# Kernel tuning notes

Measured on AMD Instinct MI355X. Metric: run time of the kernel, lower is better.

Reference implementation:

```python
import jax, jax.numpy as jnp
import numpy as np

B, T, CIN, F, K, U, FF, N, LS = 16, 384, 64, 64, 32, 128, 1024, 64, 15
EPS = 1e-3  # keras BatchNormalization epsilon

def _conv1d(x, w):
    # x:[B,T,C], w:[K,C,F], 'same' padding, no bias
    return jax.lax.conv_general_dilated(x, w, (1,), 'SAME', dimension_numbers=('NWC', 'WIO', 'NWC'))

def _bn(x, g, b, m, v):
    # inference-mode batchnorm
    return g * (x - m) * jax.lax.rsqrt(v + EPS) + b

def _gru_seq(x, k, rk, b):
    # keras GRU (reset_after=True), gate order [z, r, h]; x:[B,T,D] -> [B,T,U]
    u = rk.shape[0]
    xp = x @ k + b[0]                      # precompute input projections [B,T,3U]
    def step(h, xt):
        rec = h @ rk + b[1]
        xz, xr, xh = jnp.split(xt, 3, axis=-1)
        rz, rr_, rh = jnp.split(rec, 3, axis=-1)
        z = jax.nn.sigmoid(xz + rz)
        r = jax.nn.sigmoid(xr + rr_)
        hh = jnp.tanh(xh + r * rh)
        hn = z * h + (1.0 - z) * hh
        return hn, hn
    h0 = jnp.zeros((x.shape[0], u), x.dtype)
    _, ys = jax.lax.scan(step, h0, jnp.swapaxes(xp, 0, 1))
    return jnp.swapaxes(ys, 0, 1)

def _cgru(xr, xi, kr, rkr, br, ki, rki, bi):
    # ComplexGRUCell: real_gru applied to both parts, imag_gru applied to both parts
    rr = _gru_seq(xr, kr, rkr, br)
    ri = _gru_seq(xi, kr, rkr, br)
    ir = _gru_seq(xr, ki, rki, bi)
    ii = _gru_seq(xi, ki, rki, bi)
    return rr - ii, ri + ir

def _forward(h_real, h_imag, conv_wr, conv_wi, bn_gr, bn_br, bn_mr, bn_vr, bn_gi, bn_bi, bn_mi, bn_vi, g0_kr, g0_rkr, g0_br, g0_ki, g0_rki, g0_bi, gs_kr, gs_rkr, gs_br, gs_ki, gs_rki, gs_bi, ff1_w, ff1_b, ff2_w, ff2_b, qr_w, qr_b, qi_w, qi_b, rr_w, rr_b, ri_w, ri_b):
    xr = _bn(_conv1d(h_real, conv_wr) - _conv1d(h_imag, conv_wi), bn_gr, bn_br, bn_mr, bn_vr)
    xi = _bn(_conv1d(h_imag, conv_wr) + _conv1d(h_real, conv_wi), bn_gi, bn_bi, bn_mi, bn_vi)
    xr, xi = _cgru(xr, xi, g0_kr, g0_rkr, g0_br, g0_ki, g0_rki, g0_bi)
    for i in range(LS):  # fixed small layer count
        xr, xi = _cgru(xr, xi, gs_kr[i], gs_rkr[i], gs_br[i], gs_ki[i], gs_rki[i], gs_bi[i])
    def ff(a):
        return jax.nn.relu(a @ ff1_w + ff1_b) @ ff2_w + ff2_b
    xr = xr + ff(xr)   # dropout is identity at inference
    xi = xi + ff(xi)
    mr = jnp.mean(xr, axis=1)
    mi = jnp.mean(xi, axis=1)
    Qr = (mr @ qr_w + qr_b) - (mi @ qi_w + qi_b)
    Qi = (mi @ qr_w + qr_b) + (mr @ qi_w + qi_b)
    Rr = (mr @ rr_w + rr_b) - (mi @ ri_w + ri_b)
    Ri = (mi @ rr_w + rr_b) + (mr @ ri_w + ri_b)
    Qr = Qr.reshape(-1, N, N); Qi = Qi.reshape(-1, N, N)
    Rr = Rr.reshape(-1, N, N); Ri = Ri.reshape(-1, N, N)
    # trace(Q Q^H) = sum |Q|^2 (real, nonnegative)
    nrm = jnp.sqrt(jnp.sum(Qr * Qr + Qi * Qi, axis=(1, 2)))[:, None, None]
    scale = jnp.sqrt(jnp.float32(N)) / nrm
    return Qr * scale, Qi * scale, Rr, Ri

def setup_inputs():
    key = jax.random.key(0)
    ks = jax.random.split(key, 20)
    s = 0.05
    def nrm(k, shape, scale=s):
        return jax.random.normal(k, shape, jnp.float32) * scale
    inp = {}
    inp['h_real'] = nrm(ks[0], (B, T, CIN), 1.0)
    inp['h_imag'] = nrm(ks[1], (B, T, CIN), 1.0)
    inp['conv_wr'] = nrm(ks[2], (K, CIN, F))
    inp['conv_wi'] = nrm(ks[3], (K, CIN, F))
    for nm in ('bn_gr', 'bn_gi', 'bn_vr', 'bn_vi'):
        inp[nm] = jnp.ones((F,), jnp.float32)
    for nm in ('bn_br', 'bn_bi', 'bn_mr', 'bn_mi'):
        inp[nm] = jnp.zeros((F,), jnp.float32)
    inp['g0_kr'] = nrm(ks[4], (F, 3 * U));  inp['g0_rkr'] = nrm(ks[5], (U, 3 * U));  inp['g0_br'] = jnp.zeros((2, 3 * U), jnp.float32)
    inp['g0_ki'] = nrm(ks[6], (F, 3 * U));  inp['g0_rki'] = nrm(ks[7], (U, 3 * U));  inp['g0_bi'] = jnp.zeros((2, 3 * U), jnp.float32)
    inp['gs_kr'] = nrm(ks[8], (LS, U, 3 * U));  inp['gs_rkr'] = nrm(ks[9], (LS, U, 3 * U));  inp['gs_br'] = jnp.zeros((LS, 2, 3 * U), jnp.float32)
    inp['gs_ki'] = nrm(ks[10], (LS, U, 3 * U)); inp['gs_rki'] = nrm(ks[11], (LS, U, 3 * U)); inp['gs_bi'] = jnp.zeros((LS, 2, 3 * U), jnp.float32)
    inp['ff1_w'] = nrm(ks[12], (U, FF)); inp['ff1_b'] = jnp.zeros((FF,), jnp.float32)
    inp['ff2_w'] = nrm(ks[13], (FF, U)); inp['ff2_b'] = jnp.zeros((U,), jnp.float32)
    inp['qr_w'] = nrm(ks[14], (U, N * N)); inp['qr_b'] = jnp.zeros((N * N,), jnp.float32)
    inp['qi_w'] = nrm(ks[15], (U, N * N)); inp['qi_b'] = jnp.zeros((N * N,), jnp.float32)
    inp['rr_w'] = nrm(ks[16], (U, N * N)); inp['rr_b'] = jnp.zeros((N * N,), jnp.float32)
    inp['ri_w'] = nrm(ks[17], (U, N * N)); inp['ri_b'] = jnp.zeros((N * N,), jnp.float32)
    return inp

def reference(h_real, h_imag, conv_wr, conv_wi, bn_gr, bn_br, bn_mr, bn_vr, bn_gi, bn_bi, bn_mi, bn_vi, g0_kr, g0_rkr, g0_br, g0_ki, g0_rki, g0_bi, gs_kr, gs_rkr, gs_br, gs_ki, gs_rki, gs_bi, ff1_w, ff1_b, ff2_w, ff2_b, qr_w, qr_b, qi_w, qi_b, rr_w, rr_b, ri_w, ri_b):
    return _forward(h_real, h_imag, conv_wr, conv_wi, bn_gr, bn_br, bn_mr, bn_vr, bn_gi, bn_bi, bn_mi, bn_vi, g0_kr, g0_rkr, g0_br, g0_ki, g0_rki, g0_bi, gs_kr, gs_rkr, gs_br, gs_ki, gs_rki, gs_bi, ff1_w, ff1_b, ff2_w, ff2_b, qr_w, qr_b, qi_w, qi_b, rr_w, rr_b, ri_w, ri_b)
```

## Files before the change

kernel.cpp:

```cpp
#include <hip/hip_runtime.h>
#include <hip/hip_bf16.h>
#include <math.h>

typedef __attribute__((ext_vector_type(8))) short short8;
typedef __attribute__((ext_vector_type(4))) float f32x4;
typedef unsigned short u16;
typedef unsigned int u32;

#define CL 16
#define NCHUNK 24
#define RING 4
#define CHSZ (16*CL*128)

__device__ __forceinline__ u16 f2bf(float f){
  u32 x = __float_as_uint(f);
  u32 r = x + 0x7fffu + ((x >> 16) & 1u);
  return (u16)(r >> 16);
}
__device__ __forceinline__ float bf2f(u16 u){
  return __uint_as_float(((u32)u) << 16);
}
__device__ __forceinline__ f32x4 mfma16(short8 a, short8 b, f32x4 c){
  return __builtin_amdgcn_mfma_f32_16x16x32_bf16(a, b, c, 0, 0, 0);
}

__global__ void k_init(float* S, float* ssq, u32* Flg){
  int i = blockIdx.x*256 + threadIdx.x;
  if (i < 32768){ S[i] = 0.f; return; }
  i -= 32768;
  if (i < 16){ ssq[i] = 0.f; return; }
  i -= 16;
  if (i < 4096){ Flg[i] = 0u; return; }
}

__global__ void k_wprep(const float* __restrict__ wr, const float* __restrict__ wi,
                        const float* __restrict__ w1,
                        u16* WtR, u16* WtI, u16* WtIN, u16* W1t){
  int i = blockIdx.x*256 + threadIdx.x;
  if (i < 131072){
    int k = i >> 12, r = i & 4095, f = r >> 6, c = r & 63;
    float a = wr[(k<<12) + (c<<6) + f];
    float b = wi[(k<<12) + (c<<6) + f];
    WtR[i] = f2bf(a); WtI[i] = f2bf(b); WtIN[i] = f2bf(-b);
  } else if (i < 262144){
    int j = i - 131072;
    int col = j >> 7, k = j & 127;
    W1t[j] = f2bf(w1[(k<<10) + col]);
  }
}

__global__ __launch_bounds__(256) void k_wprep2(
    const float* __restrict__ g0_kr, const float* __restrict__ g0_ki,
    const float* __restrict__ gs_kr, const float* __restrict__ gs_ki,
    const float* __restrict__ g0_rkr, const float* __restrict__ g0_rki,
    const float* __restrict__ gs_rkr, const float* __restrict__ gs_rki,
    u16* __restrict__ KT, u16* __restrict__ RKT){
  __shared__ float tile[128][33];
  int bid = blockIdx.x;
  int ct = bid % 12; int lm = (bid/12) & 31; int which = bid / (12*32);
  int m = lm & 1, l = lm >> 1;
  int c0 = ct*32;
  int tid = threadIdx.x;
  for (int idx = tid; idx < 128*32; idx += 256){
    int k = idx >> 5, cc = idx & 31;
    float v;
    if (!which){
      if (l == 0) v = (k < 64) ? (m ? g0_ki : g0_kr)[k*384 + c0+cc] : 0.f;
      else        v = (m ? gs_ki : gs_kr)[((size_t)(l-1)*128 + k)*384 + c0+cc];
    } else {
      if (l == 0) v = (m ? g0_rki : g0_rkr)[k*384 + c0+cc];
      else        v = (m ? gs_rki : gs_rkr)[((size_t)(l-1)*128 + k)*384 + c0+cc];
    }
    tile[k][cc] = v;
  }
  __syncthreads();
  u16* dst = (which ? RKT : KT) + (size_t)lm*384*128;
  for (int idx = tid; idx < 32*128; idx += 256){
    int cc = idx >> 7, k = idx & 127;
    dst[(size_t)(c0+cc)*128 + k] = f2bf(tile[k][cc]);
  }
}

__global__ __launch_bounds__(256) void k_conv(
    const float* __restrict__ hr, const float* __restrict__ hi,
    const u16* __restrict__ WtR, const u16* __restrict__ WtI, const u16* __restrict__ WtIN,
    const float* __restrict__ gr, const float* __restrict__ gi,
    const float* __restrict__ vr, const float* __restrict__ vi,
    const float* __restrict__ br, const float* __restrict__ bi,
    const float* __restrict__ mr, const float* __restrict__ mi,
    u16* __restrict__ X0){
  __shared__ u16 xst[2*48*64];
  int tid = threadIdx.x;
  int bid = blockIdx.x;
  int b = bid / 24, t0 = (bid % 24) * 16;
  for (int el = tid; el < 2*47*64; el += 256){
    int part = el / (47*64); int rem = el % (47*64); int row = rem >> 6; int c = rem & 63;
    int tg = t0 + row - 15;
    const float* src = part ? hi : hr;
    float v = (tg >= 0 && tg < 384) ? src[((size_t)b*384 + tg)*64 + c] : 0.f;
    int idx = (part*48 + row)*64 + c;
    int byte = (idx<<1) ^ ((row&7)<<4);
    *(u16*)((char*)xst + byte) = f2bf(v);
  }
  __syncthreads();
  int lane = tid & 63, wid = tid >> 6, lr = lane & 15, lg = lane >> 4;
  f32x4 accr = {0,0,0,0}, acci = {0,0,0,0};
  for (int k = 0; k < 32; ++k){
    int row = lr + k;
    int swz = (row&7)<<4;
    for (int ch = 0; ch < 2; ++ch){
      int c0 = ch*32 + lg*8;
      int idxr = (0*48 + row)*64 + c0;
      int idxi = (1*48 + row)*64 + c0;
      short8 ar = *(const short8*)((const char*)xst + ((idxr<<1) ^ swz));
      short8 ai = *(const short8*)((const char*)xst + ((idxi<<1) ^ swz));
      size_t wb = ((size_t)(k*64 + wid*16 + lr))*64 + c0;
      short8 bwr = *(const short8*)(WtR + wb);
      short8 bwi = *(const short8*)(WtI + wb);
      short8 bwn = *(const short8*)(WtIN + wb);
      accr = mfma16(ar, bwr, accr);
      accr = mfma16(ai, bwn, accr);
      acci = mfma16(ai, bwr, acci);
      acci = mfma16(ar, bwi, acci);
    }
  }
  int f = wid*16 + lr;
  float sr_ = gr[f] * rsqrtf(vr[f] + 1e-3f), or_ = br[f] - mr[f]*sr_;
  float si_ = gi[f] * rsqrtf(vi[f] + 1e-3f), oi_ = bi[f] - mi[f]*si_;
  for (int r = 0; r < 4; ++r){
    int t = t0 + lg*4 + r;
    X0[(((size_t)0*16 + b)*384 + t)*64 + f] = f2bf(accr[r]*sr_ + or_);
    X0[(((size_t)1*16 + b)*384 + t)*64 + f] = f2bf(acci[r]*si_ + oi_);
  }
}

__global__ __launch_bounds__(512,1) void k_scanp(
    const u16* __restrict__ X0, const u16* __restrict__ KT, const u16* __restrict__ RKT,
    const float* __restrict__ g0_br, const float* __restrict__ g0_bi,
    const float* __restrict__ gs_br, const float* __restrict__ gs_bi,
    u16* __restrict__ HC, u16* __restrict__ HS15, u32* Flg)
{
  int bid = blockIdx.x;
  int l = bid >> 2, s = bid & 3;

  __shared__ u16 xs[16*CL*128];
  __shared__ u16 hs2[2*16*128];
  __shared__ float bsh[4][128];

  int tid = threadIdx.x, lane = tid & 63, wv = tid >> 6, lr = lane & 15, lg = lane >> 4;
  int m = s >> 1;

  const float* Bsrc = (l == 0) ? (m ? g0_bi : g0_br)
                               : ((m ? gs_bi : gs_br) + (size_t)(l-1)*768);
  if (tid < 128){
    int j = tid;
    bsh[0][j] = Bsrc[j]       + Bsrc[384 + j];
    bsh[1][j] = Bsrc[128 + j] + Bsrc[384 + 128 + j];
    bsh[2][j] = Bsrc[256 + j];
    bsh[3][j] = Bsrc[384 + 256 + j];
  }
  for (int i = tid; i < 2048; i += 512) ((u32*)hs2)[i] = 0u;

  const u16* Kp  = KT  + (size_t)(l*2 + m)*384*128;
  const u16* RKp = RKT + (size_t)(l*2 + m)*384*128;
  int cz = wv*16 + lr;
  short8 wz[8], wr2[8], whx[4], whr[4];
  #pragma unroll
  for (int ks = 0; ks < 4; ++ks){
    wz[ks]    = *(const short8*)(RKp + (size_t)cz*128 + ks*32 + lg*8);
    wz[4+ks]  = *(const short8*)(Kp  + (size_t)cz*128 + ks*32 + lg*8);
    wr2[ks]   = *(const short8*)(RKp + (size_t)(128+cz)*128 + ks*32 + lg*8);
    wr2[4+ks] = *(const short8*)(Kp  + (size_t)(128+cz)*128 + ks*32 + lg*8);
    whx[ks]   = *(const short8*)(Kp  + (size_t)(256+cz)*128 + ks*32 + lg*8);
    whr[ks]   = *(const short8*)(RKp + (size_t)(256+cz)*128 + ks*32 + lg*8);
  }

  float hreg[4] = {0.f, 0.f, 0.f, 0.f};

  __syncthreads();
  float bz, br_, bhx, bhr;
  {
    int j = wv*16 + lr;
    bz = bsh[0][j]; br_ = bsh[1][j]; bhx = bsh[2][j]; bhr = bsh[3][j];
  }

  u32* prodF = Flg;
  u32* consF = Flg + 2048;
  int sA = (s & 1) ? 1 : 0, sB = (s & 1) ? 2 : 3;
  int pA = (l-1)*4 + sA, pB = (l-1)*4 + sB;
  float sgn = (s & 1) ? 1.f : -1.f;
  int p = s & 1;
  int me = l*4 + s;

  for (int c = 0; c < NCHUNK; ++c){
    int t0 = c * CL;

    if (tid == 0){
      int guard = 0;
      if (l > 0){
        while (__hip_atomic_load(&prodF[pA*32], __ATOMIC_RELAXED, __HIP_MEMORY_SCOPE_AGENT) < (u32)(c+1) ||
               __hip_atomic_load(&prodF[pB*32], __ATOMIC_RELAXED, __HIP_MEMORY_SCOPE_AGENT) < (u32)(c+1)){
          __builtin_amdgcn_s_sleep(1);
          if (++guard > 10000000) break;
        }
      }
      if (l < 15 && c >= RING){
        guard = 0;
        while (__hip_atomic_load(&consF[me*32], __ATOMIC_RELAXED, __HIP_MEMORY_SCOPE_AGENT) < (u32)(2*(c-RING+1))){
          __builtin_amdgcn_s_sleep(1);
          if (++guard > 10000000) break;
        }
      }
    }
    __syncthreads();

    if (l == 0){
      for (int it = 0; it < 8; ++it){
        int g = tid + it*512;
        int k8 = g & 15, ttv = (g>>4) & 15, b = g >> 8;
        short8 v = {0,0,0,0,0,0,0,0};
        if (k8 < 8) v = *(const short8*)(X0 + (((size_t)p*16 + b)*384 + t0 + ttv)*64 + k8*8);
        int byte = (((b*CL + ttv)*128 + k8*8) << 1) ^ ((b&7)<<4);
        *(short8*)((char*)xs + byte) = v;
      }
      __syncthreads();
    } else {
      __builtin_amdgcn_fence(__ATOMIC_ACQUIRE, "agent");
      int slot = c & (RING-1);
      const u16* baseA = HC + ((size_t)pA*RING + slot)*CHSZ;
      const u16* baseB = HC + ((size_t)pB*RING + slot)*CHSZ;
      for (int it = 0; it < 8; ++it){
        int g = tid + it*512;
        int k8 = g & 15, ttv = (g>>4) & 15, b = g >> 8;
        size_t si = ((size_t)b*CL + ttv)*128 + k8*8;
        short8 va = *(const short8*)(baseA + si);
        short8 vb = *(const short8*)(baseB + si);
        short8 o;
        #pragma unroll
        for (int e = 0; e < 8; ++e){
          float f = bf2f((u16)va[e]) + sgn*bf2f((u16)vb[e]);
          o[e] = (short)f2bf(f);
        }
        int byte = (((b*CL + ttv)*128 + k8*8) << 1) ^ ((b&7)<<4);
        *(short8*)((char*)xs + byte) = o;
      }
      __syncthreads();
      if (tid == 0){
        __hip_atomic_fetch_add(&consF[pA*32], 1u, __ATOMIC_RELAXED, __HIP_MEMORY_SCOPE_AGENT);
        __hip_atomic_fetch_add(&consF[pB*32], 1u, __ATOMIC_RELAXED, __HIP_MEMORY_SCOPE_AGENT);
      }
    }

    u16* outp;
    int Tp, tbase;
    if (l < 15){
      outp = HC + ((size_t)me*RING + (c & (RING-1)))*CHSZ;
      Tp = CL; tbase = 0;
    } else {
      outp = HS15 + (size_t)s*16*384*128;
      Tp = 384; tbase = t0;
    }

    for (int q = 0; q < 4; ++q){
      f32x4 xpz[4], xpr[4], xph[4];
      #pragma unroll
      for (int t2 = 0; t2 < 4; ++t2){
        int tt = q*4 + t2;
        short8 ax[4];
        #pragma unroll
        for (int ks = 0; ks < 4; ++ks){
          int xb = (((lr*CL + tt)*128 + ks*32 + lg*8) << 1) ^ ((lr&7)<<4);
          ax[ks] = *(const short8*)((char*)xs + xb);
        }
        f32x4 az  = {bz, bz, bz, bz};
        f32x4 ar  = {br_, br_, br_, br_};
        f32x4 ahx = {bhx, bhx, bhx, bhx};
        #pragma unroll
        for (int ks = 0; ks < 4; ++ks){
          az  = mfma16(ax[ks], wz[4+ks],  az);
          ar  = mfma16(ax[ks], wr2[4+ks], ar);
          ahx = mfma16(ax[ks], whx[ks],   ahx);
        }
        xpz[t2] = az; xpr[t2] = ar; xph[t2] = ahx;
      }
      #pragma unroll
      for (int t2 = 0; t2 < 4; ++t2){
        int tt = q*4 + t2;
        int hp = tt & 1;
        short8 ah[4];
        #pragma unroll
        for (int ks = 0; ks < 4; ++ks){
          int hb = hp*4096 + (((lr*128 + ks*32 + lg*8) << 1) ^ ((lr&7)<<4));
          ah[ks] = *(const short8*)((char*)hs2 + hb);
        }
        f32x4 az  = xpz[t2];
        f32x4 ar  = xpr[t2];
        f32x4 ahr = {bhr, bhr, bhr, bhr};
        #pragma unroll
        for (int ks = 0; ks < 4; ++ks){
          az  = mfma16(ah[ks], wz[ks],  az);
          ar  = mfma16(ah[ks], wr2[ks], ar);
          ahr = mfma16(ah[ks], whr[ks], ahr);
        }
        int j = wv*16 + lr;
        #pragma unroll
        for (int r = 0; r < 4; ++r){
          int b = lg*4 + r;
          float z  = 1.f/(1.f + __expf(-az[r]));
          float rg = 1.f/(1.f + __expf(-ar[r]));
          float pre = xph[t2][r] + rg*ahr[r];
          pre = fminf(fmaxf(pre, -15.f), 15.f);
          float e2 = __expf(2.f*pre);
          float hh = (e2 - 1.f)/(e2 + 1.f);
          float hn = z*hreg[r] + (1.f - z)*hh;
          hreg[r] = hn;
          u16 hb16 = f2bf(hn);
          int byte = ((hp^1)*4096) + ((((b*128 + j) << 1)) ^ ((b&7)<<4));
          *(u16*)((char*)hs2 + byte) = hb16;
          outp[((size_t)b*Tp + tbase + tt)*128 + j] = hb16;
        }
        __syncthreads();
      }
    }

    if (l < 15 && tid == 0){
      __hip_atomic_fetch_add(&prodF[me*32], 1u, __ATOMIC_RELEASE, __HIP_MEMORY_SCOPE_AGENT);
    }
  }
}

__global__ __launch_bounds__(256) void k_ffs(const u16* __restrict__ HS, const u16* __restrict__ W1t,
                                             const float* __restrict__ b1, float* __restrict__ S){
  int bid = blockIdx.x;
  int part = bid / 384; int rem = bid % 384;
  int b = rem / 24; int rem2 = rem % 24;
  int t0 = (rem2 / 4) * 64, c0 = (rem2 % 4) * 256;
  int tid = threadIdx.x, lane = tid & 63, wid = tid >> 6, lr = lane & 15, lg = lane >> 4;
  int sA = part ? 1 : 0, sB = part ? 2 : 3;
  float sgn = part ? 1.f : -1.f;
  short8 af[4][4];
  #pragma unroll
  for (int rt = 0; rt < 4; ++rt)
    #pragma unroll
    for (int ks = 0; ks < 4; ++ks){
      size_t i1 = (((size_t)sA*16 + b)*384 + t0 + rt*16 + lr)*128 + ks*32 + lg*8;
      size_t i2 = (((size_t)sB*16 + b)*384 + t0 + rt*16 + lr)*128 + ks*32 + lg*8;
      short8 va = *(const short8*)(HS + i1);
      short8 vb = *(const short8*)(HS + i2);
      short8 o;
      #pragma unroll
      for (int e = 0; e < 8; ++e){
        float f = bf2f((u16)va[e]) + sgn*bf2f((u16)vb[e]);
        o[e] = (short)f2bf(f);
      }
      af[rt][ks] = o;
    }
  for (int ctl = 0; ctl < 4; ++ctl){
    int col = c0 + wid*64 + ctl*16 + lr;
    short8 bf[4];
    #pragma unroll
    for (int ks = 0; ks < 4; ++ks)
      bf[ks] = *(const short8*)(W1t + (size_t)col*128 + ks*32 + lg*8);
    float bias = b1[col];
    float ssum = 0.f;
    #pragma unroll
    for (int rt = 0; rt < 4; ++rt){
      f32x4 acc = {0,0,0,0};
      #pragma unroll
      for (int ks = 0; ks < 4; ++ks) acc = mfma16(af[rt][ks], bf[ks], acc);
      #pragma unroll
      for (int r = 0; r < 4; ++r) ssum += fmaxf(acc[r] + bias, 0.f);
    }
    ssum += __shfl_xor(ssum, 16, 64);
    ssum += __shfl_xor(ssum, 32, 64);
    if (lg == 0) atomicAdd(&S[((size_t)part*16 + b)*1024 + col], ssum);
  }
}

__global__ void k_mx(const u16* __restrict__ HS, float* __restrict__ Mx){
  int pb = blockIdx.x; int u = threadIdx.x;
  int p = pb >> 4, b = pb & 15;
  int sA = p ? 1 : 0, sB = p ? 2 : 3;
  float sgn = p ? 1.f : -1.f;
  float s = 0.f;
  for (int t = 0; t < 384; ++t){
    float a = bf2f(HS[(((size_t)sA*16 + b)*384 + t)*128 + u]);
    float c = bf2f(HS[(((size_t)sB*16 + b)*384 + t)*128 + u]);
    s += a + sgn*c;
  }
  Mx[pb*128 + u] = s;
}

__global__ void k_comb(const float* __restrict__ S, const float* __restrict__ Mx,
                       const float* __restrict__ w2, const float* __restrict__ b2,
                       float* __restrict__ M){
  int pb = blockIdx.x; int u = threadIdx.x;
  const float* Sp = S + (size_t)pb*1024;
  float acc = 0.f;
  for (int f = 0; f < 1024; ++f) acc += Sp[f] * w2[(size_t)f*128 + u];
  M[pb*128 + u] = Mx[pb*128 + u] * (1.f/384.f) + acc * (1.f/384.f) + b2[u];
}

__global__ __launch_bounds__(256) void k_qr(const float* __restrict__ M,
    const float* __restrict__ qr_w, const float* __restrict__ qr_b,
    const float* __restrict__ qi_w, const float* __restrict__ qi_b,
    const float* __restrict__ rr_w, const float* __restrict__ rr_b,
    const float* __restrict__ ri_w, const float* __restrict__ ri_b,
    float* __restrict__ out, float* __restrict__ ssq){
  __shared__ float smr[128], smi[128];
  int bid = blockIdx.x; int tid = threadIdx.x;
  int b = bid >> 4; int o = (bid & 15)*256 + tid;
  if (tid < 128){ smr[tid] = M[b*128 + tid]; smi[tid] = M[(16 + b)*128 + tid]; }
  __syncthreads();
  float aq=0, bq=0, cq=0, dq=0, ar=0, br2=0, cr=0, dr=0;
  for (int u = 0; u < 128; ++u){
    float mr = smr[u], mi = smi[u];
    float wqr = qr_w[(size_t)u*4096 + o], wqi = qi_w[(size_t)u*4096 + o];
    float wrr = rr_w[(size_t)u*4096 + o], wri = ri_w[(size_t)u*4096 + o];
    aq += mr*wqr;  bq += mi*wqi;  cq += mi*wqr;  dq += mr*wqi;
    ar += mr*wrr;  br2 += mi*wri; cr += mi*wrr;  dr += mr*wri;
  }
  float Qr = (aq + qr_b[o]) - (bq + qi_b[o]);
  float Qi = (cq + qr_b[o]) + (dq + qi_b[o]);
  float Rr = (ar + rr_b[o]) - (br2 + ri_b[o]);
  float Ri = (cr + rr_b[o]) + (dr + ri_b[o]);
  out[(size_t)b*4096 + o] = Qr;
  out[65536 + (size_t)b*4096 + o] = Qi;
  out[131072 + (size_t)b*4096 + o] = Rr;
  out[196608 + (size_t)b*4096 + o] = Ri;
  float ss = Qr*Qr + Qi*Qi;
  for (int off = 32; off; off >>= 1) ss += __shfl_down(ss, off, 64);
  if ((tid & 63) == 0) atomicAdd(&ssq[b], ss);
}

__global__ void k_scale(float* __restrict__ out, const float* __restrict__ ssq){
  int i = blockIdx.x*256 + threadIdx.x;
  int b = (i >> 12) & 15;
  float s = 8.f / sqrtf(ssq[b]);
  out[i] *= s;
}

extern "C" void kernel_launch(void* const* d_in, const int* in_sizes, int n_in,
                              void* d_out, int out_size, void* d_ws, size_t ws_size,
                              hipStream_t stream){
  const float* h_real = (const float*)d_in[0];
  const float* h_imag = (const float*)d_in[1];
  const float* conv_wr = (const float*)d_in[2];
  const float* conv_wi = (const float*)d_in[3];
  const float* bn_gr = (const float*)d_in[4];
  const float* bn_gi = (const float*)d_in[5];
  const float* bn_vr = (const float*)d_in[6];
  const float* bn_vi = (const float*)d_in[7];
  const float* bn_br = (const float*)d_in[8];
  const float* bn_bi = (const float*)d_in[9];
  const float* bn_mr = (const float*)d_in[10];
  const float* bn_mi = (const float*)d_in[11];
  const float* g0_kr = (const float*)d_in[12];
  const float* g0_rkr = (const float*)d_in[13];
  const float* g0_br = (const float*)d_in[14];
  const float* g0_ki = (const float*)d_in[15];
  const float* g0_rki = (const float*)d_in[16];
  const float* g0_bi = (const float*)d_in[17];
  const float* gs_kr = (const float*)d_in[18];
  const float* gs_rkr = (const float*)d_in[19];
  const float* gs_br = (const float*)d_in[20];
  const float* gs_ki = (const float*)d_in[21];
  const float* gs_rki = (const float*)d_in[22];
  const float* gs_bi = (const float*)d_in[23];
  const float* ff1_w = (const float*)d_in[24];
  const float* ff1_b = (const float*)d_in[25];
  const float* ff2_w = (const float*)d_in[26];
  const float* ff2_b = (const float*)d_in[27];
  const float* qr_w = (const float*)d_in[28];
  const float* qr_b = (const float*)d_in[29];
  const float* qi_w = (const float*)d_in[30];
  const float* qi_b = (const float*)d_in[31];
  const float* rr_w = (const float*)d_in[32];
  const float* rr_b = (const float*)d_in[33];
  const float* ri_w = (const float*)d_in[34];
  const float* ri_b = (const float*)d_in[35];

  char* ws = (char*)d_ws; size_t off = 0;
  auto carve = [&](size_t bytes)->char*{ char* p = ws + off; off += (bytes + 255) & ~(size_t)255; return p; };
  u16* X0   = (u16*)carve((size_t)2*16*384*64*2);
  u16* HC   = (u16*)carve((size_t)64*RING*CHSZ*2);
  u16* HS15 = (u16*)carve((size_t)4*16*384*128*2);
  u16* KT   = (u16*)carve((size_t)16*2*384*128*2);
  u16* RKT  = (u16*)carve((size_t)16*2*384*128*2);
  u16* WtR  = (u16*)carve(131072*2);
  u16* WtI  = (u16*)carve(131072*2);
  u16* WtIN = (u16*)carve(131072*2);
  u16* W1t  = (u16*)carve(131072*2);
  u32* Flg  = (u32*)carve(4096*4);
  float* S  = (float*)carve(32768*4);
  float* Mx = (float*)carve(4096*4);
  float* M  = (float*)carve(4096*4);
  float* ssq = (float*)carve(256);

  k_init<<<145, 256, 0, stream>>>(S, ssq, Flg);
  k_wprep<<<1024, 256, 0, stream>>>(conv_wr, conv_wi, ff1_w, WtR, WtI, WtIN, W1t);
  k_wprep2<<<768, 256, 0, stream>>>(g0_kr, g0_ki, gs_kr, gs_ki,
                                    g0_rkr, g0_rki, gs_rkr, gs_rki, KT, RKT);
  k_conv<<<384, 256, 0, stream>>>(h_real, h_imag, WtR, WtI, WtIN,
                                  bn_gr, bn_gi, bn_vr, bn_vi, bn_br, bn_bi, bn_mr, bn_mi, X0);
  k_scanp<<<64, 512, 0, stream>>>(X0, KT, RKT, g0_br, g0_bi, gs_br, gs_bi,
                                  HC, HS15, Flg);
  k_ffs<<<768, 256, 0, stream>>>(HS15, W1t, ff1_b, S);
  k_mx<<<32, 128, 0, stream>>>(HS15, Mx);
  k_comb<<<32, 128, 0, stream>>>(S, Mx, ff2_w, ff2_b, M);
  k_qr<<<256, 256, 0, stream>>>(M, qr_w, qr_b, qi_w, qi_b, rr_w, rr_b, ri_w, ri_b,
                                (float*)d_out, ssq);
  k_scale<<<512, 256, 0, stream>>>((float*)d_out, ssq);
}
```

Baseline: 1.128 ms.

## Pipeline GRU layer scan at half-chunk granularity with register prefetch and double-buffered LDS

The layer-wavefront scan kernel now hands work between layers in half-chunks of 8 timesteps instead of 16. This roughly halves the pipeline fill latency across the 16 stacked layers. The next half-chunk's inputs are loaded from global memory into registers before the current half's MFMA recurrence runs, and are written into a second LDS buffer afterward, so load latency overlaps compute. The cost is doubled shared memory for the input tile, more flag polling and syncs per chunk, and finer-grained producer/consumer counters that must stay consistent with the ring-slot reuse.

```diff
diff --git a/kernel.cpp b/kernel.cpp
--- a/kernel.cpp
+++ b/kernel.cpp
@@ -9,6 +9,7 @@
 
 #define CL 16
 #define NCHUNK 24
+#define NHALF 48
 #define RING 4
 #define CHSZ (16*CL*128)
 
@@ -143,7 +144,7 @@
   int bid = blockIdx.x;
   int l = bid >> 2, s = bid & 3;
 
-  __shared__ u16 xs[16*CL*128];
+  __shared__ u16 xs[2*16*CL*128];
   __shared__ u16 hs2[2*16*128];
   __shared__ float bsh[4][128];
 
@@ -192,19 +193,65 @@
   int p = s & 1;
   int me = l*4 + s;
 
-  for (int c = 0; c < NCHUNK; ++c){
-    int t0 = c * CL;
-
+  if (l > 0){
     if (tid == 0){
       int guard = 0;
-      if (l > 0){
-        while (__hip_atomic_load(&prodF[pA*32], __ATOMIC_RELAXED, __HIP_MEMORY_SCOPE_AGENT) < (u32)(c+1) ||
-               __hip_atomic_load(&prodF[pB*32], __ATOMIC_RELAXED, __HIP_MEMORY_SCOPE_AGENT) < (u32)(c+1)){
+      while (__hip_atomic_load(&prodF[pA*32], __ATOMIC_RELAXED, __HIP_MEMORY_SCOPE_AGENT) < 1u ||
+             __hip_atomic_load(&prodF[pB*32], __ATOMIC_RELAXED, __HIP_MEMORY_SCOPE_AGENT) < 1u){
+        __builtin_amdgcn_s_sleep(1);
+        if (++guard > 10000000) break;
+      }
+    }
+    __syncthreads();
+    __builtin_amdgcn_fence(__ATOMIC_ACQUIRE, "agent");
+    const u16* baseA = HC + ((size_t)pA*RING + 0)*CHSZ;
+    const u16* baseB = HC + ((size_t)pB*RING + 0)*CHSZ;
+    #pragma unroll
+    for (int i = 0; i < 4; ++i){
+      int g = tid + i*512;
+      int k8 = g & 15, ttl = (g>>4) & 7, b = g >> 7;
+      size_t si = ((size_t)b*CL + ttl)*128 + k8*8;
+      short8 va = *(const short8*)(baseA + si);
+      short8 vb = *(const short8*)(baseB + si);
+      short8 o;
+      #pragma unroll
+      for (int e = 0; e < 8; ++e){
+        float f = bf2f((u16)va[e]) + sgn*bf2f((u16)vb[e]);
+        o[e] = (short)f2bf(f);
+      }
+      int byte = (((b*CL + ttl)*128 + k8*8) << 1) ^ ((b&7)<<4);
+      *(short8*)((char*)xs + byte) = o;
+    }
+    __syncthreads();
+  } else {
+    #pragma unroll
+    for (int i = 0; i < 4; ++i){
+      int g = tid + i*512;
+      int k8 = g & 15, ttl = (g>>4) & 7, b = g >> 7;
+      short8 v = {0,0,0,0,0,0,0,0};
+      if (k8 < 8) v = *(const short8*)(X0 + (((size_t)p*16 + b)*384 + ttl)*64 + k8*8);
+      int byte = (((b*CL + ttl)*128 + k8*8) << 1) ^ ((b&7)<<4);
+      *(short8*)((char*)xs + byte) = v;
+    }
+    __syncthreads();
+  }
+
+  for (int k = 0; k < NHALF; ++k){
+    int c = k >> 1, h = k & 1, p2 = c & 1;
+    int m1 = k + 1;
+    int cm = m1 >> 1, hm = m1 & 1, pm = cm & 1, slm = cm & 3;
+    bool doStage = (m1 < NHALF);
+
+    if (tid == 0){
+      int guard = 0;
+      if (l > 0 && doStage){
+        while (__hip_atomic_load(&prodF[pA*32], __ATOMIC_RELAXED, __HIP_MEMORY_SCOPE_AGENT) < (u32)(m1+1) ||
+               __hip_atomic_load(&prodF[pB*32], __ATOMIC_RELAXED, __HIP_MEMORY_SCOPE_AGENT) < (u32)(m1+1)){
           __builtin_amdgcn_s_sleep(1);
           if (++guard > 10000000) break;
         }
       }
-      if (l < 15 && c >= RING){
+      if (l < 15 && h == 0 && c >= RING){
         guard = 0;
         while (__hip_atomic_load(&consF[me*32], __ATOMIC_RELAXED, __HIP_MEMORY_SCOPE_AGENT) < (u32)(2*(c-RING+1))){
           __builtin_amdgcn_s_sleep(1);
@@ -214,62 +261,46 @@
     }
     __syncthreads();
 
-    if (l == 0){
-      for (int it = 0; it < 8; ++it){
-        int g = tid + it*512;
-        int k8 = g & 15, ttv = (g>>4) & 15, b = g >> 8;
-        short8 v = {0,0,0,0,0,0,0,0};
-        if (k8 < 8) v = *(const short8*)(X0 + (((size_t)p*16 + b)*384 + t0 + ttv)*64 + k8*8);
-        int byte = (((b*CL + ttv)*128 + k8*8) << 1) ^ ((b&7)<<4);
-        *(short8*)((char*)xs + byte) = v;
-      }
-      __syncthreads();
-    } else {
-      __builtin_amdgcn_fence(__ATOMIC_ACQUIRE, "agent");
-      int slot = c & (RING-1);
-      const u16* baseA = HC + ((size_t)pA*RING + slot)*CHSZ;
-      const u16* baseB = HC + ((size_t)pB*RING + slot)*CHSZ;
-      for (int it = 0; it < 8; ++it){
-        int g = tid + it*512;
-        int k8 = g & 15, ttv = (g>>4) & 15, b = g >> 8;
-        size_t si = ((size_t)b*CL + ttv)*128 + k8*8;
-        short8 va = *(const short8*)(baseA + si);
-        short8 vb = *(const short8*)(baseB + si);
-        short8 o;
-        #pragma unroll
-        for (int e = 0; e < 8; ++e){
-          float f = bf2f((u16)va[e]) + sgn*bf2f((u16)vb[e]);
-          o[e] = (short)f2bf(f);
-        }
-        int byte = (((b*CL + ttv)*128 + k8*8) << 1) ^ ((b&7)<<4);
-        *(short8*)((char*)xs + byte) = o;
-      }
-      __syncthreads();
-      if (tid == 0){
-        __hip_atomic_fetch_add(&consF[pA*32], 1u, __ATOMIC_RELAXED, __HIP_MEMORY_SCOPE_AGENT);
-        __hip_atomic_fetch_add(&consF[pB*32], 1u, __ATOMIC_RELAXED, __HIP_MEMORY_SCOPE_AGENT);
-      }
-    }
-
-    u16* outp;
-    int Tp, tbase;
-    if (l < 15){
-      outp = HC + ((size_t)me*RING + (c & (RING-1)))*CHSZ;
-      Tp = CL; tbase = 0;
-    } else {
-      outp = HS15 + (size_t)s*16*384*128;
-      Tp = 384; tbase = t0;
-    }
-
-    for (int q = 0; q < 4; ++q){
+    short8 sva[4], svb[4];
+    if (doStage){
+      if (l > 0){
+        __builtin_amdgcn_fence(__ATOMIC_ACQUIRE, "agent");
+        const u16* baseA = HC + ((size_t)pA*RING + slm)*CHSZ;
+        const u16* baseB = HC + ((size_t)pB*RING + slm)*CHSZ;
+        #pragma unroll
+        for (int i = 0; i < 4; ++i){
+          int g = tid + i*512;
+          int k8 = g & 15, ttl = (g>>4) & 7, b = g >> 7;
+          size_t si = ((size_t)b*CL + hm*8 + ttl)*128 + k8*8;
+          sva[i] = *(const short8*)(baseA + si);
+          svb[i] = *(const short8*)(baseB + si);
+        }
+      } else {
+        int t0m = cm*CL;
+        #pragma unroll
+        for (int i = 0; i < 4; ++i){
+          int g = tid + i*512;
+          int k8 = g & 15, ttl = (g>>4) & 7, b = g >> 7;
+          short8 v = {0,0,0,0,0,0,0,0};
+          if (k8 < 8) v = *(const short8*)(X0 + (((size_t)p*16 + b)*384 + t0m + hm*8 + ttl)*64 + k8*8);
+          sva[i] = v;
+        }
+      }
+    }
+
+    u16* outp; int Tp, tbase;
+    if (l < 15){ outp = HC + ((size_t)me*RING + (c & 3))*CHSZ; Tp = CL; tbase = 0; }
+    else       { outp = HS15 + (size_t)s*16*384*128; Tp = 384; tbase = c*CL; }
+
+    for (int q2 = 0; q2 < 2; ++q2){
       f32x4 xpz[4], xpr[4], xph[4];
       #pragma unroll
       for (int t2 = 0; t2 < 4; ++t2){
-        int tt = q*4 + t2;
+        int tt = h*8 + q2*4 + t2;
         short8 ax[4];
         #pragma unroll
         for (int ks = 0; ks < 4; ++ks){
-          int xb = (((lr*CL + tt)*128 + ks*32 + lg*8) << 1) ^ ((lr&7)<<4);
+          int xb = ((((p2*16 + lr)*CL + tt)*128 + ks*32 + lg*8) << 1) ^ ((lr&7)<<4);
           ax[ks] = *(const short8*)((char*)xs + xb);
         }
         f32x4 az  = {bz, bz, bz, bz};
@@ -285,7 +316,7 @@
       }
       #pragma unroll
       for (int t2 = 0; t2 < 4; ++t2){
-        int tt = q*4 + t2;
+        int tt = h*8 + q2*4 + t2;
         int hp = tt & 1;
         short8 ah[4];
         #pragma unroll
@@ -325,6 +356,33 @@
 
     if (l < 15 && tid == 0){
       __hip_atomic_fetch_add(&prodF[me*32], 1u, __ATOMIC_RELEASE, __HIP_MEMORY_SCOPE_AGENT);
+    }
+
+    if (doStage){
+      #pragma unroll
+      for (int i = 0; i < 4; ++i){
+        int g = tid + i*512;
+        int k8 = g & 15, ttl = (g>>4) & 7, b = g >> 7;
+        int tt = hm*8 + ttl;
+        short8 o;
+        if (l > 0){
+          #pragma unroll
+          for (int e = 0; e < 8; ++e){
+            float f = bf2f((u16)sva[i][e]) + sgn*bf2f((u16)svb[i][e]);
+            o[e] = (short)f2bf(f);
+          }
+        } else {
+          o = sva[i];
+        }
+        int byte = ((((pm*16 + b)*CL + tt)*128 + k8*8) << 1) ^ ((b&7)<<4);
+        *(short8*)((char*)xs + byte) = o;
+      }
+    }
+    __syncthreads();
+
+    if (doStage && hm == 1 && l > 0 && tid == 0){
+      __hip_atomic_fetch_add(&consF[pA*32], 1u, __ATOMIC_RELAXED, __HIP_MEMORY_SCOPE_AGENT);
+      __hip_atomic_fetch_add(&consF[pB*32], 1u, __ATOMIC_RELAXED, __HIP_MEMORY_SCOPE_AGENT);
     }
   }
 }
```

After: 1.414 ms. 1.25x slower.
